# Kernel tuning notes

Measured on AMD Instinct MI355X. Metric: run time of the kernel, lower is better.

Reference implementation:

```python
import jax, jax.numpy as jnp
import numpy as np

B, T, C = 2, 2048, 2048
H = 16
ROPE_DIM, NOPE_DIM, V_DIM = 64, 64, 128
HEAD_DIM = NOPE_DIM + ROPE_DIM  # 128
Q_RANK, KV_RANK = 1536, 512


def setup_inputs() -> dict:
    key = jax.random.key(0)
    ks = jax.random.split(key, 8)
    std = 0.02
    return {
        "x": jax.random.normal(ks[0], (B, T, C), jnp.float32),
        "cos": jax.random.normal(ks[1], (1, T, 1, ROPE_DIM // 2), jnp.float32),
        "sin": jax.random.normal(ks[2], (1, T, 1, ROPE_DIM // 2), jnp.float32),
        "wq_down": jax.random.normal(ks[3], (Q_RANK, C), jnp.float32) * std,
        "wq_up": jax.random.normal(ks[4], (H * HEAD_DIM, Q_RANK), jnp.float32) * std,
        "wkv_down": jax.random.normal(ks[5], (KV_RANK, C), jnp.float32) * std,
        "wkv_up": jax.random.normal(ks[6], (H * (HEAD_DIM + V_DIM), KV_RANK), jnp.float32) * std,
        "wo": jax.random.normal(ks[7], (C, H * V_DIM), jnp.float32) * std,
    }


def _rope(x, cos, sin):
    # x: [B, T, H, rope_dim]
    d = x.shape[-1] // 2
    x1, x2 = x[..., :d], x[..., d:]
    return jnp.concatenate([x1 * cos + x2 * sin, -x1 * sin + x2 * cos], axis=-1)


def _rms_norm(x):
    eps = jnp.finfo(x.dtype).eps
    return x * jax.lax.rsqrt(jnp.mean(jnp.square(x), axis=-1, keepdims=True) + eps)


def reference(x, cos, sin, wq_down, wq_up, wkv_down, wkv_up, wo):
    # Low-rank q projection
    q = jnp.einsum('btc,rc,dr->btd', x, wq_down, wq_up)
    q = q.reshape(B, T, H, HEAD_DIM)
    q_nope, q_rope = q[..., :NOPE_DIM], q[..., NOPE_DIM:]
    # Low-rank kv projection (naive decompression)
    kv = jnp.einsum('btc,rc,dr->btd', x, wkv_down, wkv_up)
    kv = kv.reshape(B, T, H, HEAD_DIM + V_DIM)
    k_nope = kv[..., :NOPE_DIM]
    k_rope = kv[..., NOPE_DIM:HEAD_DIM]
    v = kv[..., HEAD_DIM:]
    # Partial RoPE on the rope sub-dims only
    q_rope = _rope(q_rope, cos, sin)
    k_rope = _rope(k_rope, cos, sin)
    q = _rms_norm(jnp.concatenate([q_nope, q_rope], axis=-1))
    k = _rms_norm(jnp.concatenate([k_nope, k_rope], axis=-1))
    # Causal SDPA: [B, H, T, T]
    scale = 1.0 / jnp.sqrt(jnp.float32(HEAD_DIM))
    scores = jnp.einsum('bthd,bshd->bhts', q, k) * scale
    causal = jnp.tril(jnp.ones((T, T), dtype=bool))
    scores = jnp.where(causal, scores, jnp.finfo(scores.dtype).min)
    probs = jax.nn.softmax(scores, axis=-1)
    y = jnp.einsum('bhts,bshd->bthd', probs, v).reshape(B, T, H * V_DIM)
    return y @ wo.T
```

## Files before the change

kernel.cpp:

```cpp
#include <hip/hip_runtime.h>
#include <hip/hip_bf16.h>
#include <math.h>
#include <type_traits>

#define AS1 __attribute__((address_space(1)))
#define AS3 __attribute__((address_space(3)))

typedef __bf16  bf16x8 __attribute__((ext_vector_type(8)));
typedef float   f32x4  __attribute__((ext_vector_type(4)));
typedef float   f32x16 __attribute__((ext_vector_type(16)));
typedef __hip_bfloat16 bf16;

#define MFMA16x16x32 __builtin_amdgcn_mfma_f32_16x16x32_bf16
#define MFMA32x32x16 __builtin_amdgcn_mfma_f32_32x32x16_bf16

__device__ __forceinline__ void gload16(const void* g, void* l) {
  __builtin_amdgcn_global_load_lds((const AS1 void*)g, (AS3 void*)l, 16, 0, 0);
}

struct CastArgs {
  const float4* src[6];
  ushort4* dst[6];
  unsigned bound[6];
};

__global__ __launch_bounds__(256) void f2bf_multi(CastArgs a) {
  unsigned i = blockIdx.x * 256 + threadIdx.x;
  if (i >= a.bound[5]) return;
  unsigned lo = 0;
  int s = 0;
#pragma unroll
  for (int k = 0; k < 5; k++) {
    if (i >= a.bound[k]) { s = k + 1; lo = a.bound[k]; }
  }
  unsigned idx = i - lo;
  float4 v = a.src[s][idx];
  ushort4 o;
  o.x = __builtin_bit_cast(unsigned short, __float2bfloat16(v.x));
  o.y = __builtin_bit_cast(unsigned short, __float2bfloat16(v.y));
  o.z = __builtin_bit_cast(unsigned short, __float2bfloat16(v.z));
  o.w = __builtin_bit_cast(unsigned short, __float2bfloat16(v.w));
  a.dst[s][idx] = o;
}

template <typename OutT>
__global__ __launch_bounds__(256, 3) void gemm_bt(const bf16* __restrict__ A,
                                                  const bf16* __restrict__ W,
                                                  OutT* __restrict__ Cp,
                                                  int M, int N, int K, int lda) {
  __shared__ __align__(16) bf16 As[128 * 32];
  __shared__ __align__(16) bf16 Ws[128 * 32];
  const int t = threadIdx.x;
  const int w = t >> 6, lane = t & 63;
  const int quad = lane >> 4, l16 = lane & 15;
  const int wr = (w >> 1) * 64, wc = (w & 1) * 64;
  const size_t m0 = (size_t)blockIdx.x * 128;
  const size_t n0 = (size_t)blockIdx.y * 128;

  const int rowS = t >> 2;
  const int kch  = (t & 3) * 8;

  f32x4 acc[4][4];
#pragma unroll
  for (int i = 0; i < 4; i++)
#pragma unroll
    for (int j = 0; j < 4; j++) acc[i][j] = f32x4{0.f, 0.f, 0.f, 0.f};

  for (int k0 = 0; k0 < K; k0 += 32) {
    __syncthreads();
    gload16(A + (m0 + rowS) * (size_t)lda + k0 + kch,      (char*)As + w * 1024);
    gload16(A + (m0 + rowS + 64) * (size_t)lda + k0 + kch, (char*)As + 4096 + w * 1024);
    gload16(W + (n0 + rowS) * (size_t)K + k0 + kch,        (char*)Ws + w * 1024);
    gload16(W + (n0 + rowS + 64) * (size_t)K + k0 + kch,   (char*)Ws + 4096 + w * 1024);
    __syncthreads();

    bf16x8 af[4], bw[4];
#pragma unroll
    for (int i = 0; i < 4; i++)
      af[i] = *(const bf16x8*)(As + (wr + i * 16 + l16) * 32 + quad * 8);
#pragma unroll
    for (int j = 0; j < 4; j++)
      bw[j] = *(const bf16x8*)(Ws + (wc + j * 16 + l16) * 32 + quad * 8);
#pragma unroll
    for (int i = 0; i < 4; i++)
#pragma unroll
      for (int j = 0; j < 4; j++)
        acc[i][j] = MFMA16x16x32(af[i], bw[j], acc[i][j], 0, 0, 0);
  }

#pragma unroll
  for (int i = 0; i < 4; i++)
#pragma unroll
    for (int j = 0; j < 4; j++)
#pragma unroll
      for (int r = 0; r < 4; r++) {
        size_t row = m0 + wr + i * 16 + quad * 4 + r;
        size_t col = n0 + wc + j * 16 + l16;
        float v = acc[i][j][r];
        if constexpr (std::is_same<OutT, float>::value)
          Cp[row * N + col] = v;
        else
          Cp[row * N + col] = __float2bfloat16(v);
      }
}

__global__ __launch_bounds__(256) void rope_rms(const bf16* __restrict__ qraw,
                                                const bf16* __restrict__ kvraw,
                                                const float* __restrict__ cosp,
                                                const float* __restrict__ sinp,
                                                bf16* __restrict__ qn,
                                                bf16* __restrict__ kn) {
  const int bt = blockIdx.x;
  const int w = threadIdx.x >> 6, lane = threadIdx.x & 63;
  const int h = blockIdx.y * 4 + w;
  const int tt = bt & 2047;
  const float c = cosp[tt * 32 + (lane & 31)];
  const float s = sinp[tt * 32 + (lane & 31)];
  const float inv128 = 1.0f / 128.0f;
  const float eps = 1.1920929e-7f;

  {
    const bf16* base = qraw + (size_t)bt * 2048 + h * 128;
    float a = (float)base[lane];
    float o = (float)base[64 + lane];
    float partner = __shfl_xor(o, 32);
    float orope = (lane < 32) ? (o * c + partner * s) : (o * c - partner * s);
    float ss = a * a + orope * orope;
#pragma unroll
    for (int off = 1; off < 64; off <<= 1) ss += __shfl_xor(ss, off);
    float rn = rsqrtf(ss * inv128 + eps);
    bf16* outp = qn + ((size_t)bt * 16 + h) * 128;
    outp[lane] = __float2bfloat16(a * rn);
    outp[64 + lane] = __float2bfloat16(orope * rn);
  }
  {
    const bf16* base = kvraw + (size_t)bt * 4096 + h * 256;
    float a = (float)base[lane];
    float o = (float)base[64 + lane];
    float partner = __shfl_xor(o, 32);
    float orope = (lane < 32) ? (o * c + partner * s) : (o * c - partner * s);
    float ss = a * a + orope * orope;
#pragma unroll
    for (int off = 1; off < 64; off <<= 1) ss += __shfl_xor(ss, off);
    float rn = rsqrtf(ss * inv128 + eps);
    bf16* outp = kn + ((size_t)bt * 16 + h) * 128;
    outp[lane] = __float2bfloat16(a * rn);
    outp[64 + lane] = __float2bfloat16(orope * rn);
  }
}

__global__ __launch_bounds__(256) void vtrans(const bf16* __restrict__ kvraw,
                                              bf16* __restrict__ vT) {
  __shared__ __align__(16) bf16 tile[64][72];
  const int b = blockIdx.z >> 4, h = blockIdx.z & 15;
  const int t0 = blockIdx.x * 64, d0 = blockIdx.y * 64;
  const int tr = threadIdx.x >> 2;
  const int cc = (threadIdx.x & 3) << 4;

  const bf16* src = kvraw + ((size_t)(b * 2048 + t0 + tr)) * 4096 + h * 256 + 128 + d0 + cc;
  *(uint4*)&tile[tr][cc]     = *(const uint4*)(src);
  *(uint4*)&tile[tr][cc + 8] = *(const uint4*)(src + 8);
  __syncthreads();

  __align__(16) bf16 tmp[16];
#pragma unroll
  for (int j = 0; j < 16; j++) tmp[j] = tile[cc + j][tr];
  bf16* dst = vT + ((size_t)blockIdx.z * 128 + d0 + tr) * 2048 + t0 + cc;
  *(uint4*)dst       = *(const uint4*)&tmp[0];
  *(uint4*)(dst + 8) = *(const uint4*)&tmp[8];
}

__global__ __launch_bounds__(256, 2) void attn_kernel(const bf16* __restrict__ qn,
                                                      const bf16* __restrict__ kn,
                                                      const bf16* __restrict__ vT,
                                                      bf16* __restrict__ y) {
  __shared__ __align__(16) bf16 Ks[64 * 128];
  __shared__ __align__(16) bf16 Vs[128 * 64];
  __shared__ __align__(16) bf16 Ps[4][32 * 64];
  const int t = threadIdx.x, w = t >> 6, lane = t & 63;
  const int l32 = lane & 31, hl = lane >> 5;
  const int b = blockIdx.x >> 4, h = blockIdx.x & 15;
  const int yy = blockIdx.y;
  const int xb = (yy < 8) ? (15 - yy) : (yy - 8);
  const int q0 = xb * 128;
  const int T_ = 2048, H_ = 16;

  bf16x8 qf[8];
  {
    const bf16* qbase = qn + ((size_t)(b * T_ + q0 + w * 32 + l32) * H_ + h) * 128;
#pragma unroll
    for (int ki = 0; ki < 8; ki++)
      qf[ki] = *(const bf16x8*)(qbase + (ki * 2 + hl) * 8);
  }

  f32x16 yacc[4];
#pragma unroll
  for (int db = 0; db < 4; db++)
#pragma unroll
    for (int i = 0; i < 16; i++) yacc[db][i] = 0.f;
  float lrow[16];
#pragma unroll
  for (int r = 0; r < 16; r++) lrow[r] = 0.f;
  const float K1 = 0.08838834764831845f * 1.4426950408889634f;
  const float K2 = -12.0f * 1.4426950408889634f;
  const int ntiles = 2 * xb + 2;

  for (int it = 0; it < ntiles; ++it) {
    const int s0 = it * 64;
    __syncthreads();
#pragma unroll
    for (int is = 0; is < 4; ++is) {
      int srow = is * 16 + w * 4 + (lane >> 4);
      int cg = (lane & 15) ^ (srow & 7);
      gload16(kn + ((size_t)(b * T_ + s0 + srow) * H_ + h) * 128 + cg * 8,
              (char*)Ks + is * 4096 + w * 1024);
    }
#pragma unroll
    for (int is = 0; is < 4; ++is) {
      int drow = is * 32 + w * 8 + (lane >> 3);
      int cg = (lane & 7) ^ (drow & 7);
      gload16(vT + ((size_t)(b * H_ + h) * 128 + drow) * T_ + s0 + cg * 8,
              (char*)Vs + is * 4096 + w * 1024);
    }
    __syncthreads();

    f32x16 sacc[2];
#pragma unroll
    for (int cb = 0; cb < 2; cb++)
#pragma unroll
      for (int i = 0; i < 16; i++) sacc[cb][i] = 0.f;
#pragma unroll
    for (int cb = 0; cb < 2; ++cb) {
      const int s = cb * 32 + l32;
#pragma unroll
      for (int ki = 0; ki < 8; ++ki) {
        int pos = (ki * 2 + hl) ^ (s & 7);
        bf16x8 kf = *(const bf16x8*)(Ks + s * 128 + pos * 8);
        sacc[cb] = MFMA32x32x16(qf[ki], kf, sacc[cb], 0, 0, 0);
      }
    }

    const bool diag = (it >= ntiles - 2);
#pragma unroll
    for (int cb = 0; cb < 2; ++cb) {
      const int sidx = cb * 32 + l32;
      const int sg = s0 + sidx;
#pragma unroll
      for (int r = 0; r < 16; ++r) {
        const int row = (r & 3) + 8 * (r >> 2) + 4 * hl;
        float e;
        if (diag && (sg > q0 + w * 32 + row))
          e = 0.0f;
        else
          e = exp2f(fmaf(sacc[cb][r], K1, K2));
        lrow[r] += e;
        Ps[w][row * 64 + (((sidx >> 3) ^ (row & 7)) << 3) + (sidx & 7)] =
            __float2bfloat16(e);
      }
    }
    __asm__ volatile("s_waitcnt lgkmcnt(0)" ::: "memory");

#pragma unroll
    for (int ki = 0; ki < 4; ++ki) {
      int ppos = (ki * 2 + hl) ^ (l32 & 7);
      bf16x8 pf = *(const bf16x8*)(&Ps[w][l32 * 64 + ppos * 8]);
#pragma unroll
      for (int db = 0; db < 4; ++db) {
        int d = db * 32 + l32;
        int vpos = (ki * 2 + hl) ^ (d & 7);
        bf16x8 vf = *(const bf16x8*)(Vs + d * 64 + vpos * 8);
        yacc[db] = MFMA32x32x16(pf, vf, yacc[db], 0, 0, 0);
      }
    }
  }

#pragma unroll
  for (int r = 0; r < 16; r++) {
#pragma unroll
    for (int off = 1; off < 32; off <<= 1) lrow[r] += __shfl_xor(lrow[r], off);
  }
#pragma unroll
  for (int r = 0; r < 16; r++) {
    const int row = (r & 3) + 8 * (r >> 2) + 4 * hl;
    float inv = 1.0f / lrow[r];
    size_t qrow = (size_t)(b * T_ + q0 + w * 32 + row);
    bf16* outp = y + qrow * 2048 + h * 128;
#pragma unroll
    for (int db = 0; db < 4; db++)
      outp[db * 32 + l32] = __float2bfloat16(yacc[db][r] * inv);
  }
}

extern "C" void kernel_launch(void* const* d_in, const int* in_sizes, int n_in,
                              void* d_out, int out_size, void* d_ws, size_t ws_size,
                              hipStream_t stream) {
  (void)in_sizes; (void)n_in; (void)out_size; (void)ws_size;
  const float* x    = (const float*)d_in[0];
  const float* cosp = (const float*)d_in[1];
  const float* sinp = (const float*)d_in[2];
  const float* wqd  = (const float*)d_in[3];
  const float* wqu  = (const float*)d_in[4];
  const float* wkvd = (const float*)d_in[5];
  const float* wkvu = (const float*)d_in[6];
  const float* wo   = (const float*)d_in[7];
  float* out = (float*)d_out;

  char* ws = (char*)d_ws;
  size_t off = 0;
  auto alloc = [&](size_t elems) { bf16* p = (bf16*)(ws + off); off += elems * 2; return p; };
  bf16* xb      = alloc((size_t)4096 * 2048);
  bf16* wqdB    = alloc((size_t)1536 * 2048);
  bf16* wkvdB   = alloc((size_t)512 * 2048);
  bf16* wquB    = alloc((size_t)2048 * 1536);
  bf16* wkvuB   = alloc((size_t)4096 * 512);
  bf16* woB     = alloc((size_t)2048 * 2048);
  bf16* qkvdown = alloc((size_t)4096 * 2048);
  bf16* qraw    = alloc((size_t)4096 * 2048);
  bf16* kvraw   = alloc((size_t)4096 * 4096);
  bf16* qnb     = alloc((size_t)4096 * 16 * 128);
  bf16* knb     = alloc((size_t)4096 * 16 * 128);
  bf16* vTb     = alloc((size_t)2 * 16 * 128 * 2048);
  bf16* yb      = alloc((size_t)4096 * 2048);

  CastArgs ca;
  const float* srcs[6] = {x, wqd, wkvd, wqu, wkvu, wo};
  bf16* dsts[6]        = {xb, wqdB, wkvdB, wquB, wkvuB, woB};
  size_t cnts[6] = {(size_t)4096 * 2048, (size_t)1536 * 2048, (size_t)512 * 2048,
                    (size_t)2048 * 1536, (size_t)4096 * 512,  (size_t)2048 * 2048};
  unsigned cum = 0;
  for (int i = 0; i < 6; i++) {
    ca.src[i] = (const float4*)srcs[i];
    ca.dst[i] = (ushort4*)dsts[i];
    cum += (unsigned)(cnts[i] / 4);
    ca.bound[i] = cum;
  }
  f2bf_multi<<<dim3((cum + 255) / 256), 256, 0, stream>>>(ca);

  gemm_bt<bf16><<<dim3(32, 16), 256, 0, stream>>>(xb, wqdB, qkvdown, 4096, 2048, 2048, 2048);
  gemm_bt<bf16><<<dim3(32, 16), 256, 0, stream>>>(qkvdown, wquB, qraw, 4096, 2048, 1536, 2048);
  gemm_bt<bf16><<<dim3(32, 32), 256, 0, stream>>>(qkvdown + 1536, wkvuB, kvraw, 4096, 4096, 512, 2048);
  rope_rms<<<dim3(4096, 4), 256, 0, stream>>>(qraw, kvraw, cosp, sinp, qnb, knb);
  vtrans<<<dim3(32, 2, 32), 256, 0, stream>>>(kvraw, vTb);
  attn_kernel<<<dim3(32, 16), 256, 0, stream>>>(qnb, knb, vTb, yb);
  gemm_bt<float><<<dim3(32, 16), 256, 0, stream>>>(yb, woB, out, 4096, 2048, 2048, 2048);
}
```

Before: 391.5 us.

## Fuse V transpose into kv-up GEMM epilogue and shrink attention blocks to 64 queries

Adds a specialized kv-up GEMM whose epilogue writes the V half of each head directly in transposed [b,h,d,t] layout. This removes the separate vtrans kernel and its read and write of V. Attention blocks are also halved to 2 waves covering 64 query rows, doubling the grid and reordering the causal schedule for finer load balance. The trade-off is strided 8-byte transposed stores in the GEMM epilogue and lower per-block reuse of K/V tiles in attention.

```diff
diff --git a/kernel.cpp b/kernel.cpp
--- a/kernel.cpp
+++ b/kernel.cpp
@@ -16,6 +16,10 @@
 
 __device__ __forceinline__ void gload16(const void* g, void* l) {
   __builtin_amdgcn_global_load_lds((const AS1 void*)g, (AS3 void*)l, 16, 0, 0);
+}
+
+__device__ __forceinline__ unsigned short bfbits(float v) {
+  return __builtin_bit_cast(unsigned short, __float2bfloat16(v));
 }
 
 struct CastArgs {
@@ -36,10 +40,7 @@
   unsigned idx = i - lo;
   float4 v = a.src[s][idx];
   ushort4 o;
-  o.x = __builtin_bit_cast(unsigned short, __float2bfloat16(v.x));
-  o.y = __builtin_bit_cast(unsigned short, __float2bfloat16(v.y));
-  o.z = __builtin_bit_cast(unsigned short, __float2bfloat16(v.z));
-  o.w = __builtin_bit_cast(unsigned short, __float2bfloat16(v.w));
+  o.x = bfbits(v.x); o.y = bfbits(v.y); o.z = bfbits(v.z); o.w = bfbits(v.w);
   a.dst[s][idx] = o;
 }
 
@@ -56,7 +57,6 @@
   const int wr = (w >> 1) * 64, wc = (w & 1) * 64;
   const size_t m0 = (size_t)blockIdx.x * 128;
   const size_t n0 = (size_t)blockIdx.y * 128;
-
   const int rowS = t >> 2;
   const int kch  = (t & 3) * 8;
 
@@ -102,6 +102,81 @@
         else
           Cp[row * N + col] = __float2bfloat16(v);
       }
+}
+
+__global__ __launch_bounds__(256, 3) void gemm_kvup(const bf16* __restrict__ A,
+                                                    const bf16* __restrict__ W,
+                                                    bf16* __restrict__ kvraw,
+                                                    bf16* __restrict__ vT) {
+  __shared__ __align__(16) bf16 As[128 * 32];
+  __shared__ __align__(16) bf16 Ws[128 * 32];
+  const int t = threadIdx.x;
+  const int w = t >> 6, lane = t & 63;
+  const int quad = lane >> 4, l16 = lane & 15;
+  const int wr = (w >> 1) * 64, wc = (w & 1) * 64;
+  const size_t m0 = (size_t)blockIdx.x * 128;
+  const int n0 = (int)blockIdx.y * 128;
+  const int rowS = t >> 2;
+  const int kch  = (t & 3) * 8;
+  const int K = 512, lda = 2048;
+
+  f32x4 acc[4][4];
+#pragma unroll
+  for (int i = 0; i < 4; i++)
+#pragma unroll
+    for (int j = 0; j < 4; j++) acc[i][j] = f32x4{0.f, 0.f, 0.f, 0.f};
+
+  for (int k0 = 0; k0 < K; k0 += 32) {
+    __syncthreads();
+    gload16(A + (m0 + rowS) * (size_t)lda + k0 + kch,        (char*)As + w * 1024);
+    gload16(A + (m0 + rowS + 64) * (size_t)lda + k0 + kch,   (char*)As + 4096 + w * 1024);
+    gload16(W + ((size_t)n0 + rowS) * K + k0 + kch,          (char*)Ws + w * 1024);
+    gload16(W + ((size_t)n0 + rowS + 64) * K + k0 + kch,     (char*)Ws + 4096 + w * 1024);
+    __syncthreads();
+
+    bf16x8 af[4], bw[4];
+#pragma unroll
+    for (int i = 0; i < 4; i++)
+      af[i] = *(const bf16x8*)(As + (wr + i * 16 + l16) * 32 + quad * 8);
+#pragma unroll
+    for (int j = 0; j < 4; j++)
+      bw[j] = *(const bf16x8*)(Ws + (wc + j * 16 + l16) * 32 + quad * 8);
+#pragma unroll
+    for (int i = 0; i < 4; i++)
+#pragma unroll
+      for (int j = 0; j < 4; j++)
+        acc[i][j] = MFMA16x16x32(af[i], bw[j], acc[i][j], 0, 0, 0);
+  }
+
+  if ((n0 & 128) == 0) {
+#pragma unroll
+    for (int i = 0; i < 4; i++)
+#pragma unroll
+      for (int j = 0; j < 4; j++)
+#pragma unroll
+        for (int r = 0; r < 4; r++) {
+          size_t row = m0 + wr + i * 16 + quad * 4 + r;
+          size_t col = (size_t)n0 + wc + j * 16 + l16;
+          kvraw[row * 4096 + col] = __float2bfloat16(acc[i][j][r]);
+        }
+  } else {
+    const int h = n0 >> 8;
+#pragma unroll
+    for (int i = 0; i < 4; i++) {
+      size_t row = m0 + wr + i * 16 + quad * 4;
+      int bb = (int)(row >> 11), tloc = (int)(row & 2047);
+#pragma unroll
+      for (int j = 0; j < 4; j++) {
+        int d = wc + j * 16 + l16;
+        ushort4 v4;
+        v4.x = bfbits(acc[i][j][0]);
+        v4.y = bfbits(acc[i][j][1]);
+        v4.z = bfbits(acc[i][j][2]);
+        v4.w = bfbits(acc[i][j][3]);
+        *(ushort4*)(vT + ((size_t)(bb * 16 + h) * 128 + d) * 2048 + tloc) = v4;
+      }
+    }
+  }
 }
 
 __global__ __launch_bounds__(256) void rope_rms(const bf16* __restrict__ qraw,
@@ -149,40 +224,24 @@
   }
 }
 
-__global__ __launch_bounds__(256) void vtrans(const bf16* __restrict__ kvraw,
-                                              bf16* __restrict__ vT) {
-  __shared__ __align__(16) bf16 tile[64][72];
-  const int b = blockIdx.z >> 4, h = blockIdx.z & 15;
-  const int t0 = blockIdx.x * 64, d0 = blockIdx.y * 64;
-  const int tr = threadIdx.x >> 2;
-  const int cc = (threadIdx.x & 3) << 4;
-
-  const bf16* src = kvraw + ((size_t)(b * 2048 + t0 + tr)) * 4096 + h * 256 + 128 + d0 + cc;
-  *(uint4*)&tile[tr][cc]     = *(const uint4*)(src);
-  *(uint4*)&tile[tr][cc + 8] = *(const uint4*)(src + 8);
-  __syncthreads();
-
-  __align__(16) bf16 tmp[16];
-#pragma unroll
-  for (int j = 0; j < 16; j++) tmp[j] = tile[cc + j][tr];
-  bf16* dst = vT + ((size_t)blockIdx.z * 128 + d0 + tr) * 2048 + t0 + cc;
-  *(uint4*)dst       = *(const uint4*)&tmp[0];
-  *(uint4*)(dst + 8) = *(const uint4*)&tmp[8];
-}
-
-__global__ __launch_bounds__(256, 2) void attn_kernel(const bf16* __restrict__ qn,
+__global__ __launch_bounds__(128, 2) void attn_kernel(const bf16* __restrict__ qn,
                                                       const bf16* __restrict__ kn,
                                                       const bf16* __restrict__ vT,
                                                       bf16* __restrict__ y) {
   __shared__ __align__(16) bf16 Ks[64 * 128];
   __shared__ __align__(16) bf16 Vs[128 * 64];
-  __shared__ __align__(16) bf16 Ps[4][32 * 64];
+  __shared__ __align__(16) bf16 Ps[2][32 * 64];
   const int t = threadIdx.x, w = t >> 6, lane = t & 63;
   const int l32 = lane & 31, hl = lane >> 5;
   const int b = blockIdx.x >> 4, h = blockIdx.x & 15;
-  const int yy = blockIdx.y;
-  const int xb = (yy < 8) ? (15 - yy) : (yy - 8);
-  const int q0 = xb * 128;
+  const int yy = (int)blockIdx.y;
+  const int y0 = yy & 7, k4 = yy >> 3;
+  int xb;
+  if (k4 == 0) xb = 31 - y0;
+  else if (k4 == 1) xb = y0;
+  else if (k4 == 2) xb = 23 - y0;
+  else xb = 8 + y0;
+  const int q0 = xb * 64;
   const int T_ = 2048, H_ = 16;
 
   bf16x8 qf[8];
@@ -190,7 +249,7 @@
     const bf16* qbase = qn + ((size_t)(b * T_ + q0 + w * 32 + l32) * H_ + h) * 128;
 #pragma unroll
     for (int ki = 0; ki < 8; ki++)
-      qf[ki] = *(const bf16x8*)(qbase + (ki * 2 + hl) * 8);
+      qf[ki] = *(const bf16x8*)(qbase + ki * 16 + hl * 8);
   }
 
   f32x16 yacc[4];
@@ -203,24 +262,26 @@
   for (int r = 0; r < 16; r++) lrow[r] = 0.f;
   const float K1 = 0.08838834764831845f * 1.4426950408889634f;
   const float K2 = -12.0f * 1.4426950408889634f;
-  const int ntiles = 2 * xb + 2;
+  const int ntiles = xb + 1;
 
   for (int it = 0; it < ntiles; ++it) {
     const int s0 = it * 64;
     __syncthreads();
 #pragma unroll
-    for (int is = 0; is < 4; ++is) {
-      int srow = is * 16 + w * 4 + (lane >> 4);
+    for (int is = 0; is < 8; ++is) {
+      int i = is * 2 + w;
+      int srow = i * 4 + (lane >> 4);
       int cg = (lane & 15) ^ (srow & 7);
       gload16(kn + ((size_t)(b * T_ + s0 + srow) * H_ + h) * 128 + cg * 8,
-              (char*)Ks + is * 4096 + w * 1024);
-    }
-#pragma unroll
-    for (int is = 0; is < 4; ++is) {
-      int drow = is * 32 + w * 8 + (lane >> 3);
+              (char*)Ks + i * 1024);
+    }
+#pragma unroll
+    for (int is = 0; is < 8; ++is) {
+      int i = is * 2 + w;
+      int drow = i * 8 + (lane >> 3);
       int cg = (lane & 7) ^ (drow & 7);
       gload16(vT + ((size_t)(b * H_ + h) * 128 + drow) * T_ + s0 + cg * 8,
-              (char*)Vs + is * 4096 + w * 1024);
+              (char*)Vs + i * 1024);
     }
     __syncthreads();
 
@@ -240,7 +301,7 @@
       }
     }
 
-    const bool diag = (it >= ntiles - 2);
+    const bool diag = (it == xb);
 #pragma unroll
     for (int cb = 0; cb < 2; ++cb) {
       const int sidx = cb * 32 + l32;
@@ -338,9 +399,8 @@
 
   gemm_bt<bf16><<<dim3(32, 16), 256, 0, stream>>>(xb, wqdB, qkvdown, 4096, 2048, 2048, 2048);
   gemm_bt<bf16><<<dim3(32, 16), 256, 0, stream>>>(qkvdown, wquB, qraw, 4096, 2048, 1536, 2048);
-  gemm_bt<bf16><<<dim3(32, 32), 256, 0, stream>>>(qkvdown + 1536, wkvuB, kvraw, 4096, 4096, 512, 2048);
+  gemm_kvup<<<dim3(32, 32), 256, 0, stream>>>(qkvdown + 1536, wkvuB, kvraw, vTb);
   rope_rms<<<dim3(4096, 4), 256, 0, stream>>>(qraw, kvraw, cosp, sinp, qnb, knb);
-  vtrans<<<dim3(32, 2, 32), 256, 0, stream>>>(kvraw, vTb);
-  attn_kernel<<<dim3(32, 16), 256, 0, stream>>>(qnb, knb, vTb, yb);
+  attn_kernel<<<dim3(32, 32), 128, 0, stream>>>(qnb, knb, vTb, yb);
   gemm_bt<float><<<dim3(32, 16), 256, 0, stream>>>(yb, woB, out, 4096, 2048, 2048, 2048);
 }
```

Measured after the change: 393.8 us. No clear change (+0.6%).
